# Kernel tuning notes

Hardware: AMD Instinct MI355X
Metric: run time of the kernel (lower is better)

Reference implementation:

```python
import jax, jax.numpy as jnp
import numpy as np

EPS = 1e-5

def _ln(x, g, b):
    m = x.mean(-1, keepdims=True)
    v = ((x - m) ** 2).mean(-1, keepdims=True)
    return (x - m) / jnp.sqrt(v + EPS) * g + b

def _mlp(x, W0, b0, W1, b1, g, b):
    # Linear -> SiLU -> Linear -> LayerNorm (GraphCast MLP, num_layers=1)
    h = jax.nn.silu(x @ W0 + b0)
    return _ln(h @ W1 + b1, g, b)

NG, NM, E, D, H = 65536, 40962, 196608, 512, 512

def setup_inputs() -> dict:
    key = jax.random.key(0)
    ks = jax.random.split(key, 16)
    def lin(k, i, o):
        return (jax.random.normal(k, (i, o), jnp.float32) / np.sqrt(i)).astype(jnp.float32)
    inp = {
        "grid_nfeat": jax.random.normal(ks[0], (NG, D), jnp.float32),
        "mesh_nfeat": jax.random.normal(ks[1], (NM, D), jnp.float32),
        "edge_index": jax.random.randint(ks[2], (2, E), 0, NM),
        "mesh2grid_efeat": jax.random.normal(ks[3], (E, 4), jnp.float32),
        # decoder embedder MLP: 4 -> H -> D, LayerNorm
        "emb_W0": lin(ks[4], 4, H), "emb_b0": jnp.zeros(H, jnp.float32),
        "emb_W1": lin(ks[5], H, D), "emb_b1": jnp.zeros(D, jnp.float32),
        "emb_g": jnp.ones(D, jnp.float32), "emb_b": jnp.zeros(D, jnp.float32),
        # interaction-net edge MLP: concat(e, src, dst) = 3D -> H -> D, LayerNorm
        "edge_W0": lin(ks[6], 3 * D, H), "edge_b0": jnp.zeros(H, jnp.float32),
        "edge_W1": lin(ks[7], H, D), "edge_b1": jnp.zeros(D, jnp.float32),
        "edge_g": jnp.ones(D, jnp.float32), "edge_beta": jnp.zeros(D, jnp.float32),
        # interaction-net node MLP: concat(dst, agg) = 2D -> H -> D, LayerNorm
        "node_W0": lin(ks[8], 2 * D, H), "node_b0": jnp.zeros(H, jnp.float32),
        "node_W1": lin(ks[9], H, D), "node_b1": jnp.zeros(D, jnp.float32),
        "node_g": jnp.ones(D, jnp.float32), "node_beta": jnp.zeros(D, jnp.float32),
    }
    return inp

def reference(grid_nfeat, mesh_nfeat, edge_index, mesh2grid_efeat,
              emb_W0, emb_b0, emb_W1, emb_b1, emb_g, emb_b,
              edge_W0, edge_b0, edge_W1, edge_b1, edge_g, edge_beta,
              node_W0, node_b0, node_W1, node_b1, node_g, node_beta):
    # 1) embed raw mesh2grid edge features [E,4] -> [E,D]
    e = _mlp(mesh2grid_efeat, emb_W0, emb_b0, emb_W1, emb_b1, emb_g, emb_b)
    src = edge_index[0]  # mesh sender node ids
    dst = edge_index[1]  # grid receiver node ids
    # 2) edge update: gather sender (mesh) / receiver (grid) feats, MLP, residual
    e_in = jnp.concatenate([e, mesh_nfeat[src], grid_nfeat[dst]], axis=-1)  # [E,3D]
    e_new = _mlp(e_in, edge_W0, edge_b0, edge_W1, edge_b1, edge_g, edge_beta) + e
    # 3) scatter-sum messages to grid nodes, node MLP, residual
    agg = jax.ops.segment_sum(e_new, dst, num_segments=grid_nfeat.shape[0])  # [NG,D]
    n_in = jnp.concatenate([grid_nfeat, agg], axis=-1)  # [NG,2D]
    n_new = _mlp(n_in, node_W0, node_b0, node_W1, node_b1, node_g, node_beta) + grid_nfeat
    return n_new
```

## Files before the change

kernel.cpp:

```cpp
#include <hip/hip_runtime.h>
#include <hip/hip_fp16.h>
#include <math.h>


#define NG 65536
#define NM 40962
#define NE 196608

using f16   = _Float16;
using f16x8 = __attribute__((ext_vector_type(8))) _Float16;
using f16x4 = __attribute__((ext_vector_type(4))) _Float16;
using f32x4 = __attribute__((ext_vector_type(4))) float;


__global__ void cvt_rows_kernel(const float* __restrict__ in, f16* __restrict__ out, int n4) {
    int stride = gridDim.x * blockDim.x;
    for (int i = blockIdx.x * blockDim.x + threadIdx.x; i < n4; i += stride) {
        float4 v = ((const float4*)in)[i];
        f16x4 o; o[0] = (f16)v.x; o[1] = (f16)v.y; o[2] = (f16)v.z; o[3] = (f16)v.w;
        ((f16x4*)out)[i] = o;
    }
}

__global__ void transpose_w_kernel(const float* __restrict__ W, f16* __restrict__ WT, int K) {
    int total = K * 512;
    int stride = gridDim.x * blockDim.x;
    for (int idx = blockIdx.x * blockDim.x + threadIdx.x; idx < total; idx += stride) {
        int k = idx % K;
        int c = idx / K;
        WT[idx] = (f16)W[(size_t)k * 512 + c];
    }
}


__global__ void count_kernel(const int* __restrict__ dst, int* __restrict__ counts) {
    int i = blockIdx.x * 256 + threadIdx.x;
    if (i < NE) atomicAdd(&counts[dst[i]], 1);
}

__global__ void scan_kernel(const int* __restrict__ counts, int* __restrict__ offs,
                            int* __restrict__ cursor) {
    __shared__ int part[1024];
    int t = threadIdx.x;
    int base = t * 64;
    int loc[64];
    int s = 0;
    #pragma unroll
    for (int i = 0; i < 64; ++i) { loc[i] = s; s += counts[base + i]; }
    part[t] = s;
    __syncthreads();
    for (int off = 1; off < 1024; off <<= 1) {
        int v = (t >= off) ? part[t - off] : 0;
        __syncthreads();
        part[t] += v;
        __syncthreads();
    }
    int pre = (t == 0) ? 0 : part[t - 1];
    #pragma unroll
    for (int i = 0; i < 64; ++i) { int o = pre + loc[i]; offs[base + i] = o; cursor[base + i] = o; }
    if (t == 1023) offs[65536] = pre + s;
}

__global__ void fill_kernel(const int* __restrict__ dst, int* __restrict__ cursor,
                            int* __restrict__ perm) {
    int i = blockIdx.x * 256 + threadIdx.x;
    if (i < NE) {
        int d = dst[i];
        int p = atomicAdd(&cursor[d], 1);
        perm[p] = i;
    }
}


__global__ void agg_kernel(const f16* __restrict__ enew,
                           const int* __restrict__ offs,
                           const int* __restrict__ perm,
                           f16* __restrict__ agg) {
    int node = blockIdx.x * 4 + (threadIdx.x >> 6);
    int lane = threadIdx.x & 63;
    int beg = offs[node], end = offs[node + 1];
    float a[8] = {0.f, 0.f, 0.f, 0.f, 0.f, 0.f, 0.f, 0.f};
    for (int j = beg; j < end; ++j) {
        int e = perm[j];
        f16x8 v = *(const f16x8*)(enew + (size_t)e * 512 + lane * 8);
        #pragma unroll
        for (int i = 0; i < 8; ++i) a[i] += (float)v[i];
    }
    f16x8 o;
    #pragma unroll
    for (int i = 0; i < 8; ++i) o[i] = (f16)a[i];
    *(f16x8*)(agg + (size_t)node * 512 + lane * 8) = o;
}


template <int MODE>
__global__ __launch_bounds__(512, 2) __attribute__((flatten))
void mlp_fused(const float* __restrict__ xin,
               const f16*  eA,
               const f16*  __restrict__ meshA,
               const f16*  __restrict__ gridA,
               const int*  __restrict__ srcIdx,
               const int*  __restrict__ dstIdx,
               const float* __restrict__ W0emb,
               const f16*  __restrict__ W0T,
               const float* __restrict__ b0,
               const f16*  __restrict__ W1T,
               const float* __restrict__ b1,
               const float* __restrict__ gma,
               const float* __restrict__ bta,
               const float* __restrict__ resF32,
               float* __restrict__ outF32,
               f16*  outF16)
{
    constexpr int K1  = (MODE == 1) ? 1536 : (MODE == 2 ? 1024 : 64);
    constexpr int NS1 = (MODE == 0) ? 0 : K1 / 64;

    __shared__ __align__(16) f16 hbuf[64 * 512];
    __shared__ __align__(16) f16 btile[512 * 64];
    __shared__ __align__(16) f16 atile[64 * 64];
    __shared__ float red1[64][8];
    __shared__ float red2[64][8];
    __shared__ float mrow[64];
    __shared__ float rrow[64];
    __shared__ float xemb[256];

    const int tid  = threadIdx.x;
    const int lane = tid & 63;
    const int w    = tid >> 6;
    const int l15  = lane & 15;
    const int lg   = lane >> 4;
    const int row0 = blockIdx.x * 64;

    const int ar   = tid >> 3;
    const int ap   = tid & 7;
    const int aswz = ap ^ (ar & 7);

    int rid = 0, sid = 0, did = 0;
    if constexpr (MODE == 1 || MODE == 2) rid = row0 + ar;
    if constexpr (MODE == 1) { sid = srcIdx[rid]; did = dstIdx[rid]; }

    auto ldB = [&](const f16* WT, int K, int s, f16x8 (&b_)[8]) {
        const int k0 = s * 64;
        #pragma unroll
        for (int q = 0; q < 8; ++q)
            b_[q] = *(const f16x8*)(WT + (size_t)(q * 64 + ar) * K + (k0 + ap * 8));
    };
    auto ldA1 = [&](int s, f16x8& a_) {
        const int k0 = s * 64;
        if constexpr (MODE == 1) {
            const f16* p;
            if (k0 < 512)       p = eA    + (size_t)rid * 512 + (k0 + ap * 8);
            else if (k0 < 1024) p = meshA + (size_t)sid * 512 + (k0 - 512 + ap * 8);
            else                p = gridA + (size_t)did * 512 + (k0 - 1024 + ap * 8);
            a_ = *(const f16x8*)p;
        } else if constexpr (MODE == 2) {
            const f16* p = (k0 < 512)
                ? (gridA + (size_t)rid * 512 + (k0 + ap * 8))
                : (meshA + (size_t)rid * 512 + (k0 - 512 + ap * 8));
            a_ = *(const f16x8*)p;
        }
    };

    f16x8 cvA[8], cvB[8];
    if constexpr (MODE == 0) ldB(W1T, 512, 0, cvA);

    f16x8 avA, avB, bvA[8], bvB[8];
    if constexpr (MODE == 1 || MODE == 2) { ldA1(0, avA); ldB(W0T, K1, 0, bvA); }

    if constexpr (MODE == 0) {
        if (tid < 256) xemb[tid] = xin[(size_t)row0 * 4 + tid];
        __syncthreads();
        const int c = tid;
        float w0c0 = W0emb[c], w0c1 = W0emb[512 + c], w0c2 = W0emb[1024 + c], w0c3 = W0emb[1536 + c];
        float b0c = b0[c];
        const int cs = c >> 3, c7 = c & 7;
        #pragma unroll 4
        for (int r = 0; r < 64; ++r) {
            float v = b0c;
            v = fmaf(xemb[r * 4 + 0], w0c0, v);
            v = fmaf(xemb[r * 4 + 1], w0c1, v);
            v = fmaf(xemb[r * 4 + 2], w0c2, v);
            v = fmaf(xemb[r * 4 + 3], w0c3, v);
            v = v / (1.f + __expf(-v));
            hbuf[r * 512 + ((cs ^ (r & 7)) * 8) + c7] = (f16)v;
        }
    }

    f32x4 acc2[4][4] = {};
    if constexpr (MODE == 1 || MODE == 2) {
        f32x4 acc[4][4] = {};

        auto step1 = [&](int s, f16x8& aC, f16x8 (&bC)[8], f16x8& aN, f16x8 (&bN)[8]) {
            __syncthreads();
            *(f16x8*)&atile[ar * 64 + aswz * 8] = aC;
            #pragma unroll
            for (int q = 0; q < 8; ++q)
                *(f16x8*)&btile[(q * 64 + ar) * 64 + aswz * 8] = bC[q];
            __syncthreads();

            if (s + 1 < NS1) { ldA1(s + 1, aN); ldB(W0T, K1, s + 1, bN); }

            #pragma unroll
            for (int ks = 0; ks < 2; ++ks) {
                const int ch = ks * 4 + lg;
                f16x8 af[4];
                #pragma unroll
                for (int rf = 0; rf < 4; ++rf) {
                    int r = rf * 16 + l15;
                    af[rf] = *(const f16x8*)&atile[r * 64 + ((ch ^ (r & 7)) * 8)];
                }
                #pragma unroll
                for (int cf = 0; cf < 4; ++cf) {
                    int c = w * 64 + cf * 16 + l15;
                    f16x8 bf = *(const f16x8*)&btile[c * 64 + ((ch ^ (c & 7)) * 8)];
                    #pragma unroll
                    for (int rf = 0; rf < 4; ++rf)
                        acc[rf][cf] = __builtin_amdgcn_mfma_f32_16x16x32_f16(af[rf], bf, acc[rf][cf], 0, 0, 0);
                }
            }
        };

        #pragma unroll 1
        for (int s = 0; s < NS1; s += 2) {
            step1(s,     avA, bvA, avB, bvB);
            step1(s + 1, avB, bvB, avA, bvA);
        }

        ldB(W1T, 512, 0, cvA);

        float b0c[4];
        #pragma unroll
        for (int cf = 0; cf < 4; ++cf) b0c[cf] = b0[w * 64 + cf * 16 + l15];
        #pragma unroll
        for (int rf = 0; rf < 4; ++rf)
            #pragma unroll
            for (int i = 0; i < 4; ++i) {
                int r = rf * 16 + lg * 4 + i;
                #pragma unroll
                for (int cf = 0; cf < 4; ++cf) {
                    int c = w * 64 + cf * 16 + l15;
                    float v = acc[rf][cf][i] + b0c[cf];
                    v = v / (1.f + __expf(-v));
                    hbuf[r * 512 + (((c >> 3) ^ (r & 7)) * 8) + (c & 7)] = (f16)v;
                }
            }
    }

    {
        auto step2 = [&](int s, f16x8 (&cC)[8], f16x8 (&cN)[8]) {
            __syncthreads();
            #pragma unroll
            for (int q = 0; q < 8; ++q)
                *(f16x8*)&btile[(q * 64 + ar) * 64 + aswz * 8] = cC[q];
            __syncthreads();

            if (s < 7) ldB(W1T, 512, s + 1, cN);

            #pragma unroll
            for (int ks = 0; ks < 2; ++ks) {
                const int chb = s * 8 + ks * 4 + lg;
                const int ch  = ks * 4 + lg;
                f16x8 af[4];
                #pragma unroll
                for (int rf = 0; rf < 4; ++rf) {
                    int r = rf * 16 + l15;
                    af[rf] = *(const f16x8*)&hbuf[r * 512 + ((chb ^ (r & 7)) * 8)];
                }
                #pragma unroll
                for (int cf = 0; cf < 4; ++cf) {
                    int c = w * 64 + cf * 16 + l15;
                    f16x8 bf = *(const f16x8*)&btile[c * 64 + ((ch ^ (c & 7)) * 8)];
                    #pragma unroll
                    for (int rf = 0; rf < 4; ++rf)
                        acc2[rf][cf] = __builtin_amdgcn_mfma_f32_16x16x32_f16(af[rf], bf, acc2[rf][cf], 0, 0, 0);
                }
            }
        };

        #pragma unroll 1
        for (int s = 0; s < 8; s += 2) {
            step2(s,     cvA, cvB);
            step2(s + 1, cvB, cvA);
        }

        float b1c[4], gc[4], bc[4];
        #pragma unroll
        for (int cf = 0; cf < 4; ++cf) {
            int c = w * 64 + cf * 16 + l15;
            b1c[cf] = b1[c]; gc[cf] = gma[c]; bc[cf] = bta[c];
        }
        #pragma unroll
        for (int rf = 0; rf < 4; ++rf)
            #pragma unroll
            for (int cf = 0; cf < 4; ++cf)
                #pragma unroll
                for (int i = 0; i < 4; ++i)
                    acc2[rf][cf][i] += b1c[cf];

        #pragma unroll
        for (int rf = 0; rf < 4; ++rf)
            #pragma unroll
            for (int i = 0; i < 4; ++i) {
                float p1 = 0.f, p2 = 0.f;
                #pragma unroll
                for (int cf = 0; cf < 4; ++cf) { float v = acc2[rf][cf][i]; p1 += v; p2 += v * v; }
                #pragma unroll
                for (int m = 1; m < 16; m <<= 1) { p1 += __shfl_xor(p1, m); p2 += __shfl_xor(p2, m); }
                if (l15 == 0) { int r = rf * 16 + lg * 4 + i; red1[r][w] = p1; red2[r][w] = p2; }
            }
        __syncthreads();
        if (tid < 64) {
            float s1 = 0.f, s2 = 0.f;
            #pragma unroll
            for (int ww = 0; ww < 8; ++ww) { s1 += red1[tid][ww]; s2 += red2[tid][ww]; }
            float mean = s1 * (1.f / 512.f);
            float var  = s2 * (1.f / 512.f) - mean * mean;
            mrow[tid] = mean;
            rrow[tid] = 1.f / sqrtf(var + 1e-5f);
        }
        __syncthreads();

        #pragma unroll
        for (int rf = 0; rf < 4; ++rf)
            #pragma unroll
            for (int i = 0; i < 4; ++i) {
                int r = rf * 16 + lg * 4 + i;
                float mean = mrow[r], rs = rrow[r];
                size_t grow = (size_t)(row0 + r);
                #pragma unroll
                for (int cf = 0; cf < 4; ++cf) {
                    int c = w * 64 + cf * 16 + l15;
                    float v = (acc2[rf][cf][i] - mean) * rs * gc[cf] + bc[cf];
                    if constexpr (MODE == 0) {
                        outF16[grow * 512 + c] = (f16)v;
                    } else if constexpr (MODE == 1) {
                        v += (float)eA[grow * 512 + c];
                        outF16[grow * 512 + c] = (f16)v;
                    } else {
                        v += resF32[grow * 512 + c];
                        outF32[grow * 512 + c] = v;
                    }
                }
            }
    }
}


extern "C" void kernel_launch(void* const* d_in, const int* in_sizes, int n_in,
                              void* d_out, int out_size, void* d_ws, size_t ws_size,
                              hipStream_t stream) {
    (void)in_sizes; (void)n_in; (void)out_size; (void)ws_size;

    const float* grid_nfeat = (const float*)d_in[0];
    const float* mesh_nfeat = (const float*)d_in[1];
    const int*   edge_index = (const int*)d_in[2];
    const float* efeat      = (const float*)d_in[3];
    const float* emb_W0 = (const float*)d_in[4];
    const float* emb_b0 = (const float*)d_in[5];
    const float* emb_W1 = (const float*)d_in[6];
    const float* emb_b1 = (const float*)d_in[7];
    const float* emb_g  = (const float*)d_in[8];
    const float* emb_b  = (const float*)d_in[9];
    const float* edge_W0 = (const float*)d_in[10];
    const float* edge_b0 = (const float*)d_in[11];
    const float* edge_W1 = (const float*)d_in[12];
    const float* edge_b1 = (const float*)d_in[13];
    const float* edge_g  = (const float*)d_in[14];
    const float* edge_bt = (const float*)d_in[15];
    const float* node_W0 = (const float*)d_in[16];
    const float* node_b0 = (const float*)d_in[17];
    const float* node_W1 = (const float*)d_in[18];
    const float* node_b1 = (const float*)d_in[19];
    const float* node_g  = (const float*)d_in[20];
    const float* node_bt = (const float*)d_in[21];

    const int* srcIdx = edge_index;
    const int* dstIdx = edge_index + NE;

    char* ws = (char*)d_ws;
    size_t off = 0;
    auto alloc = [&](size_t bytes) {
        void* p = ws + off;
        off += (bytes + 255) & ~(size_t)255;
        return p;
    };
    f16* grid_f16 = (f16*)alloc((size_t)NG * 512 * 2);
    f16* mesh_f16 = (f16*)alloc((size_t)NM * 512 * 2);
    f16* e_f16    = (f16*)alloc((size_t)NE * 512 * 2);
    f16* agg_f16  = (f16*)alloc((size_t)NG * 512 * 2);
    f16* w_emb1T  = (f16*)alloc((size_t)512 * 512 * 2);
    f16* w_edge0T = (f16*)alloc((size_t)512 * 1536 * 2);
    f16* w_edge1T = (f16*)alloc((size_t)512 * 512 * 2);
    f16* w_node0T = (f16*)alloc((size_t)512 * 1024 * 2);
    f16* w_node1T = (f16*)alloc((size_t)512 * 512 * 2);
    int* counts = (int*)alloc((size_t)NG * 4);
    int* offs   = (int*)alloc((size_t)(NG + 1) * 4);
    int* cursor = (int*)alloc((size_t)NG * 4);
    int* perm   = (int*)alloc((size_t)NE * 4);

    hipMemsetAsync(counts, 0, (size_t)NG * 4, stream);
    cvt_rows_kernel<<<2048, 256, 0, stream>>>(grid_nfeat, grid_f16, NG * 512 / 4);
    cvt_rows_kernel<<<2048, 256, 0, stream>>>(mesh_nfeat, mesh_f16, NM * 512 / 4);
    transpose_w_kernel<<<512, 256, 0, stream>>>(emb_W1,  w_emb1T,  512);
    transpose_w_kernel<<<512, 256, 0, stream>>>(edge_W0, w_edge0T, 1536);
    transpose_w_kernel<<<512, 256, 0, stream>>>(edge_W1, w_edge1T, 512);
    transpose_w_kernel<<<512, 256, 0, stream>>>(node_W0, w_node0T, 1024);
    transpose_w_kernel<<<512, 256, 0, stream>>>(node_W1, w_node1T, 512);
    count_kernel<<<NE / 256, 256, 0, stream>>>(dstIdx, counts);
    scan_kernel<<<1, 1024, 0, stream>>>(counts, offs, cursor);
    fill_kernel<<<NE / 256, 256, 0, stream>>>(dstIdx, cursor, perm);

    mlp_fused<0><<<NE / 64, 512, 0, stream>>>(
        efeat, nullptr, nullptr, nullptr, nullptr, nullptr,
        emb_W0, nullptr, emb_b0, w_emb1T, emb_b1, emb_g, emb_b,
        nullptr, nullptr, e_f16);

    mlp_fused<1><<<NE / 64, 512, 0, stream>>>(
        nullptr, e_f16, mesh_f16, grid_f16, srcIdx, dstIdx,
        nullptr, w_edge0T, edge_b0, w_edge1T, edge_b1, edge_g, edge_bt,
        nullptr, nullptr, e_f16);

    agg_kernel<<<NG / 4, 256, 0, stream>>>(e_f16, offs, perm, agg_f16);

    mlp_fused<2><<<NG / 64, 512, 0, stream>>>(
        nullptr, nullptr, agg_f16, grid_f16, nullptr, nullptr,
        nullptr, w_node0T, node_b0, w_node1T, node_b1, node_g, node_bt,
        grid_nfeat, (float*)d_out, nullptr);
}
```

Measured before the change: 1.773 ms.

## Process edges in dst-sorted order, deepen prefetch, swizzle block order, tile weight transpose

Edges are now processed in destination-sorted order. The embedding MLP reads its raw features through perm, and the edge MLP uses sorted src/dst arrays, so the aggregation kernel reads e_new contiguously with no indirection. The main MLP loops prefetch two K-steps ahead instead of one, and block indices are remapped with an XCD-style interleave. Weight transposes now use a shared-memory tiled kernel for coalesced reads and writes. The cost is extra index arrays and higher register pressure from the deeper prefetch.

New measurement: 1.763 ms. No clear change (-0.6%).

```diff
diff --git a/kernel.cpp b/kernel.cpp
--- a/kernel.cpp
+++ b/kernel.cpp
@@ -23,12 +23,22 @@
 }
 
 __global__ void transpose_w_kernel(const float* __restrict__ W, f16* __restrict__ WT, int K) {
-    int total = K * 512;
-    int stride = gridDim.x * blockDim.x;
-    for (int idx = blockIdx.x * blockDim.x + threadIdx.x; idx < total; idx += stride) {
-        int k = idx % K;
-        int c = idx / K;
-        WT[idx] = (f16)W[(size_t)k * 512 + c];
+    __shared__ f16 t[64][66];
+    const int nkb = K >> 6;
+    const int kb = (blockIdx.x % nkb) << 6;
+    const int cb = (blockIdx.x / nkb) << 6;
+    const int tx = threadIdx.x & 63;
+    const int ty = threadIdx.x >> 6;
+    #pragma unroll
+    for (int i = 0; i < 16; ++i) {
+        int r = i * 4 + ty;
+        t[r][tx] = (f16)W[(size_t)(kb + r) * 512 + (cb + tx)];
+    }
+    __syncthreads();
+    #pragma unroll
+    for (int i = 0; i < 16; ++i) {
+        int c = i * 4 + ty;
+        WT[(size_t)(cb + c) * K + (kb + tx)] = t[tx][c];
     }
 }
 
@@ -61,28 +71,29 @@
     if (t == 1023) offs[65536] = pre + s;
 }
 
-__global__ void fill_kernel(const int* __restrict__ dst, int* __restrict__ cursor,
-                            int* __restrict__ perm) {
+__global__ void fill_kernel(const int* __restrict__ src, const int* __restrict__ dst,
+                            int* __restrict__ cursor, int* __restrict__ perm,
+                            int* __restrict__ srcs, int* __restrict__ dsts) {
     int i = blockIdx.x * 256 + threadIdx.x;
     if (i < NE) {
         int d = dst[i];
         int p = atomicAdd(&cursor[d], 1);
         perm[p] = i;
+        srcs[p] = src[i];
+        dsts[p] = d;
     }
 }
 
 
 __global__ void agg_kernel(const f16* __restrict__ enew,
                            const int* __restrict__ offs,
-                           const int* __restrict__ perm,
                            f16* __restrict__ agg) {
     int node = blockIdx.x * 4 + (threadIdx.x >> 6);
     int lane = threadIdx.x & 63;
     int beg = offs[node], end = offs[node + 1];
     float a[8] = {0.f, 0.f, 0.f, 0.f, 0.f, 0.f, 0.f, 0.f};
     for (int j = beg; j < end; ++j) {
-        int e = perm[j];
-        f16x8 v = *(const f16x8*)(enew + (size_t)e * 512 + lane * 8);
+        f16x8 v = *(const f16x8*)(enew + (size_t)j * 512 + lane * 8);
         #pragma unroll
         for (int i = 0; i < 8; ++i) a[i] += (float)v[i];
     }
@@ -101,6 +112,7 @@
                const f16*  __restrict__ gridA,
                const int*  __restrict__ srcIdx,
                const int*  __restrict__ dstIdx,
+               const int*  __restrict__ permIdx,
                const float* __restrict__ W0emb,
                const f16*  __restrict__ W0T,
                const float* __restrict__ b0,
@@ -129,7 +141,10 @@
     const int w    = tid >> 6;
     const int l15  = lane & 15;
     const int lg   = lane >> 4;
-    const int row0 = blockIdx.x * 64;
+
+    const int cpx  = (int)gridDim.x >> 3;
+    const int bid  = ((int)blockIdx.x & 7) * cpx + ((int)blockIdx.x >> 3);
+    const int row0 = bid * 64;
 
     const int ar   = tid >> 3;
     const int ap   = tid & 7;
@@ -162,13 +177,22 @@
     };
 
     f16x8 cvA[8], cvB[8];
-    if constexpr (MODE == 0) ldB(W1T, 512, 0, cvA);
+    if constexpr (MODE == 0) {
+        ldB(W1T, 512, 0, cvA);
+        ldB(W1T, 512, 1, cvB);
+    }
 
     f16x8 avA, avB, bvA[8], bvB[8];
-    if constexpr (MODE == 1 || MODE == 2) { ldA1(0, avA); ldB(W0T, K1, 0, bvA); }
+    if constexpr (MODE == 1 || MODE == 2) {
+        ldA1(0, avA); ldB(W0T, K1, 0, bvA);
+        ldA1(1, avB); ldB(W0T, K1, 1, bvB);
+    }
 
     if constexpr (MODE == 0) {
-        if (tid < 256) xemb[tid] = xin[(size_t)row0 * 4 + tid];
+        if (tid < 256) {
+            int pr = permIdx[row0 + (tid >> 2)];
+            xemb[tid] = xin[(size_t)pr * 4 + (tid & 3)];
+        }
         __syncthreads();
         const int c = tid;
         float w0c0 = W0emb[c], w0c1 = W0emb[512 + c], w0c2 = W0emb[1024 + c], w0c3 = W0emb[1536 + c];
@@ -190,7 +214,7 @@
     if constexpr (MODE == 1 || MODE == 2) {
         f32x4 acc[4][4] = {};
 
-        auto step1 = [&](int s, f16x8& aC, f16x8 (&bC)[8], f16x8& aN, f16x8 (&bN)[8]) {
+        auto step1 = [&](int s, f16x8& aC, f16x8 (&bC)[8]) {
             __syncthreads();
             *(f16x8*)&atile[ar * 64 + aswz * 8] = aC;
             #pragma unroll
@@ -198,7 +222,7 @@
                 *(f16x8*)&btile[(q * 64 + ar) * 64 + aswz * 8] = bC[q];
             __syncthreads();
 
-            if (s + 1 < NS1) { ldA1(s + 1, aN); ldB(W0T, K1, s + 1, bN); }
+            if (s + 2 < NS1) { ldA1(s + 2, aC); ldB(W0T, K1, s + 2, bC); }
 
             #pragma unroll
             for (int ks = 0; ks < 2; ++ks) {
@@ -222,11 +246,12 @@
 
         #pragma unroll 1
         for (int s = 0; s < NS1; s += 2) {
-            step1(s,     avA, bvA, avB, bvB);
-            step1(s + 1, avB, bvB, avA, bvA);
+            step1(s,     avA, bvA);
+            step1(s + 1, avB, bvB);
         }
 
         ldB(W1T, 512, 0, cvA);
+        ldB(W1T, 512, 1, cvB);
 
         float b0c[4];
         #pragma unroll
@@ -247,14 +272,14 @@
     }
 
     {
-        auto step2 = [&](int s, f16x8 (&cC)[8], f16x8 (&cN)[8]) {
+        auto step2 = [&](int s, f16x8 (&cC)[8]) {
             __syncthreads();
             #pragma unroll
             for (int q = 0; q < 8; ++q)
                 *(f16x8*)&btile[(q * 64 + ar) * 64 + aswz * 8] = cC[q];
             __syncthreads();
 
-            if (s < 7) ldB(W1T, 512, s + 1, cN);
+            if (s + 2 < 8) ldB(W1T, 512, s + 2, cC);
 
             #pragma unroll
             for (int ks = 0; ks < 2; ++ks) {
@@ -279,8 +304,8 @@
 
         #pragma unroll 1
         for (int s = 0; s < 8; s += 2) {
-            step2(s,     cvA, cvB);
-            step2(s + 1, cvB, cvA);
+            step2(s,     cvA);
+            step2(s + 1, cvB);
         }
 
         float b1c[4], gc[4], bc[4];
@@ -397,33 +422,35 @@
     int* offs   = (int*)alloc((size_t)(NG + 1) * 4);
     int* cursor = (int*)alloc((size_t)NG * 4);
     int* perm   = (int*)alloc((size_t)NE * 4);
+    int* srcs   = (int*)alloc((size_t)NE * 4);
+    int* dsts   = (int*)alloc((size_t)NE * 4);
 
     hipMemsetAsync(counts, 0, (size_t)NG * 4, stream);
     cvt_rows_kernel<<<2048, 256, 0, stream>>>(grid_nfeat, grid_f16, NG * 512 / 4);
     cvt_rows_kernel<<<2048, 256, 0, stream>>>(mesh_nfeat, mesh_f16, NM * 512 / 4);
-    transpose_w_kernel<<<512, 256, 0, stream>>>(emb_W1,  w_emb1T,  512);
-    transpose_w_kernel<<<512, 256, 0, stream>>>(edge_W0, w_edge0T, 1536);
-    transpose_w_kernel<<<512, 256, 0, stream>>>(edge_W1, w_edge1T, 512);
-    transpose_w_kernel<<<512, 256, 0, stream>>>(node_W0, w_node0T, 1024);
-    transpose_w_kernel<<<512, 256, 0, stream>>>(node_W1, w_node1T, 512);
+    transpose_w_kernel<<<(512 / 64) * 8,  256, 0, stream>>>(emb_W1,  w_emb1T,  512);
+    transpose_w_kernel<<<(1536 / 64) * 8, 256, 0, stream>>>(edge_W0, w_edge0T, 1536);
+    transpose_w_kernel<<<(512 / 64) * 8,  256, 0, stream>>>(edge_W1, w_edge1T, 512);
+    transpose_w_kernel<<<(1024 / 64) * 8, 256, 0, stream>>>(node_W0, w_node0T, 1024);
+    transpose_w_kernel<<<(512 / 64) * 8,  256, 0, stream>>>(node_W1, w_node1T, 512);
     count_kernel<<<NE / 256, 256, 0, stream>>>(dstIdx, counts);
     scan_kernel<<<1, 1024, 0, stream>>>(counts, offs, cursor);
-    fill_kernel<<<NE / 256, 256, 0, stream>>>(dstIdx, cursor, perm);
+    fill_kernel<<<NE / 256, 256, 0, stream>>>(srcIdx, dstIdx, cursor, perm, srcs, dsts);
 
     mlp_fused<0><<<NE / 64, 512, 0, stream>>>(
-        efeat, nullptr, nullptr, nullptr, nullptr, nullptr,
+        efeat, nullptr, nullptr, nullptr, nullptr, nullptr, perm,
         emb_W0, nullptr, emb_b0, w_emb1T, emb_b1, emb_g, emb_b,
         nullptr, nullptr, e_f16);
 
     mlp_fused<1><<<NE / 64, 512, 0, stream>>>(
-        nullptr, e_f16, mesh_f16, grid_f16, srcIdx, dstIdx,
+        nullptr, e_f16, mesh_f16, grid_f16, srcs, dsts, nullptr,
         nullptr, w_edge0T, edge_b0, w_edge1T, edge_b1, edge_g, edge_bt,
         nullptr, nullptr, e_f16);
 
-    agg_kernel<<<NG / 4, 256, 0, stream>>>(e_f16, offs, perm, agg_f16);
+    agg_kernel<<<NG / 4, 256, 0, stream>>>(e_f16, offs, agg_f16);
 
     mlp_fused<2><<<NG / 64, 512, 0, stream>>>(
-        nullptr, nullptr, agg_f16, grid_f16, nullptr, nullptr,
+        nullptr, nullptr, agg_f16, grid_f16, nullptr, nullptr, nullptr,
         nullptr, w_node0T, node_b0, w_node1T, node_b1, node_g, node_bt,
         grid_nfeat, (float*)d_out, nullptr);
 }
```
